# Kernel optimization log

Measured on AMD Instinct MI355X. Metric: run time of the kernel, lower is better.

Reference implementation:

```python
import jax, jax.numpy as jnp
import numpy as np

N_NODES = 64
N_EDGES = N_NODES * (N_NODES - 1)  # 4032 (fully connected, no self-loops)
BATCH = 64
N_IN = 64
N_HID = 128
N_OUT = 16


def _linear_params(key, fan_in, fan_out):
    # mimic torch nn.Linear default init: U(-1/sqrt(fan_in), 1/sqrt(fan_in))
    kw, kb = jax.random.split(key)
    s = 1.0 / np.sqrt(fan_in)
    W = jax.random.uniform(kw, (fan_in, fan_out), minval=-s, maxval=s, dtype=jnp.float32)
    b = jax.random.uniform(kb, (fan_out,), minval=-s, maxval=s, dtype=jnp.float32)
    return W, b


def setup_inputs() -> dict:
    key = jax.random.key(0)
    ks = jax.random.split(key, 10)
    # one-hot relation matrices for fully-connected graph without self loops
    pairs = np.array([(i, j) for i in range(N_NODES) for j in range(N_NODES) if i != j])
    eye = np.eye(N_NODES, dtype=np.float32)
    rel_send = jnp.asarray(eye[pairs[:, 0]])  # [E, N]
    rel_rec = jnp.asarray(eye[pairs[:, 1]])   # [E, N]

    x = jax.random.normal(ks[0], (BATCH, N_NODES, N_IN), dtype=jnp.float32)

    w1a, b1a = _linear_params(ks[1], N_IN, N_HID)
    w1b, b1b = _linear_params(ks[2], N_HID, N_HID)
    w2a, b2a = _linear_params(ks[3], 2 * N_HID, N_HID)
    w2b, b2b = _linear_params(ks[4], N_HID, N_HID)
    w3a, b3a = _linear_params(ks[5], N_HID, N_HID)
    w3b, b3b = _linear_params(ks[6], N_HID, N_HID)
    w4a, b4a = _linear_params(ks[7], 3 * N_HID, N_HID)  # factor=True
    w4b, b4b = _linear_params(ks[8], N_HID, N_HID)
    wout, bout = _linear_params(ks[9], N_HID, N_OUT)

    return dict(x=x, rel_rec=rel_rec, rel_send=rel_send,
                w1a=w1a, b1a=b1a, w1b=w1b, b1b=b1b,
                w2a=w2a, b2a=b2a, w2b=w2b, b2b=b2b,
                w3a=w3a, b3a=b3a, w3b=w3b, b3b=b3b,
                w4a=w4a, b4a=b4a, w4b=w4b, b4b=b4b,
                wout=wout, bout=bout)


def _mlp(x, wa, ba, wb, bb):
    # Linear -> ReLU -> Linear
    return jax.nn.relu(x @ wa + ba) @ wb + bb


def reference(x, rel_rec, rel_send,
              w1a, b1a, w1b, b1b,
              w2a, b2a, w2b, b2b,
              w3a, b3a, w3b, b3b,
              w4a, b4a, w4b, b4b,
              wout, bout):
    def node2edge(h):
        receivers = jnp.einsum('en,bnh->beh', rel_rec, h)
        senders = jnp.einsum('en,bnh->beh', rel_send, h)
        return jnp.concatenate([senders, receivers], axis=-1)  # [B,E,2H]

    def edge2node(e):
        agg = jnp.einsum('en,beh->bnh', rel_rec, e)
        norm = rel_rec.sum(0)[None, :, None]  # [1,N,1]
        return agg / (norm + 1e-6)

    h = _mlp(x, w1a, b1a, w1b, b1b)            # [B,N,H]
    e = _mlp(node2edge(h), w2a, b2a, w2b, b2b)  # [B,E,H]
    x_skip = e
    # factor=True branch
    n = _mlp(edge2node(e), w3a, b3a, w3b, b3b)  # [B,N,H]
    e2 = node2edge(n)                           # [B,E,2H]
    e2 = jnp.concatenate([e2, x_skip], axis=2)  # [B,E,3H]
    e2 = _mlp(e2, w4a, b4a, w4b, b4b)           # [B,E,H]
    return e2 @ wout + bout                     # [B,E,n_out]
```

## Files before the change

### kernel.cpp

```cpp
#include <hip/hip_runtime.h>
#include <hip/hip_bf16.h>


#define DI __device__ __forceinline__

typedef short bf16x8 __attribute__((ext_vector_type(8)));
typedef float f32x4 __attribute__((ext_vector_type(4)));
typedef unsigned short u16;

static constexpr int NN = 64, NE = 4032, H = 128;

DI u16 f2bf(float f) {
  union { float f; unsigned u; } v; v.f = f;
  unsigned u = v.u;
  return (u16)((u + 0x7fffu + ((u >> 16) & 1u)) >> 16);
}
DI unsigned pk2(float a, float b) {
  union { __hip_bfloat162 h; unsigned u; } c;
  c.h = __float22bfloat162_rn(float2{a, b});
  return c.u;
}
DI f32x4 mf(bf16x8 a, bf16x8 b, f32x4 c) {
  return __builtin_amdgcn_mfma_f32_16x16x32_bf16(a, b, c, 0, 0, 0);
}
DI bf16x8 ldfrag(const u16* __restrict__ p, int idx, int l) {
  return *reinterpret_cast<const bf16x8*>(p + (idx * 64 + l) * 8);
}

__global__ __launch_bounds__(64) void prepack_kernel(
    const float* __restrict__ w1a, const float* __restrict__ w1b,
    const float* __restrict__ w2a, const float* __restrict__ w2b,
    const float* __restrict__ w3a, const float* __restrict__ w3b,
    const float* __restrict__ w4a, const float* __restrict__ w4b,
    const float* __restrict__ wout,
    const float* __restrict__ b2b, const float* __restrict__ b4b,
    const float* __restrict__ bout,
    u16* __restrict__ pk, float* __restrict__ c2, float* __restrict__ c4) {
  int seg = blockIdx.y, f = blockIdx.x, l = threadIdx.x;
  int h = l >> 4, mm = l & 15;
  if (seg == 10) {
    if (f >= 4) return;
    union { u16 u[8]; uint4 q; } o;
#pragma unroll
    for (int jj = 0; jj < 8; jj++) {
      int row = f * 32 + (jj >> 2) * 16 + h * 4 + (jj & 3);
      float s = 0.f;
      for (int j = 0; j < 128; j++) s += w4b[row * 128 + j] * wout[j * 16 + mm];
      o.u[jj] = f2bf(s);
    }
    *reinterpret_cast<uint4*>(pk + ((304 + f) * 64 + l) * 8) = o.q;
    return;
  }
  if (seg == 11) {
    if (f < 2) {
      int o = f * 64 + l;
      float s = 0.f;
      for (int k = 0; k < 128; k++) s += b2b[k] * w4a[(256 + k) * 128 + o];
      c2[o] = s;
    } else if (f == 2 && l < 16) {
      float s = bout[l];
      for (int k = 0; k < 128; k++) s += b4b[k] * wout[k * 16 + l];
      c4[l] = s;
    }
    return;
  }
  const float* src; int foff, nfrag, roff, pi;
  switch (seg) {
    case 0:  src = w1a; foff = 0;   nfrag = 16; roff = 0;   pi = 0; break;
    case 1:  src = w1b; foff = 16;  nfrag = 32; roff = 0;   pi = 1; break;
    case 2:  src = w2a; foff = 48;  nfrag = 32; roff = 0;   pi = 1; break;
    case 3:  src = w2a; foff = 80;  nfrag = 32; roff = 128; pi = 1; break;
    case 4:  src = w2b; foff = 112; nfrag = 32; roff = 0;   pi = 0; break;
    case 5:  src = w3a; foff = 144; nfrag = 32; roff = 0;   pi = 1; break;
    case 6:  src = w3b; foff = 176; nfrag = 32; roff = 0;   pi = 1; break;
    case 7:  src = w4a; foff = 208; nfrag = 32; roff = 0;   pi = 1; break;
    case 8:  src = w4a; foff = 240; nfrag = 32; roff = 128; pi = 1; break;
    default: src = w4a; foff = 272; nfrag = 32; roff = 256; pi = 1; break;
  }
  if (f >= nfrag) return;
  int kt = f >> 3, ct = f & 7;
  union { u16 u[8]; uint4 q; } o;
#pragma unroll
  for (int jj = 0; jj < 8; jj++) {
    int row = pi ? (kt * 32 + (jj >> 2) * 16 + h * 4 + (jj & 3))
                 : (kt * 32 + h * 8 + jj);
    o.u[jj] = f2bf(src[(roff + row) * 128 + ct * 16 + mm]);
  }
  *reinterpret_cast<uint4*>(pk + ((foff + f) * 64 + l) * 8) = o.q;
}

__global__ __launch_bounds__(256, 4) void node_kernel(
    const float* __restrict__ x, const u16* __restrict__ pk,
    const float* __restrict__ b1a, const float* __restrict__ b1b,
    const float* __restrict__ b2a,
    float* __restrict__ sproj, float* __restrict__ rproj) {
  __shared__ bf16x8 act[2][4][64];
  int blk = blockIdx.x, b = blk >> 2, nq = blk & 3;
  int tid = threadIdx.x, l = tid & 63, w = tid >> 6;
  int m = l & 15, h = l >> 4;
  int node = nq * 16 + m;
  const f32x4 Z = {0.f, 0.f, 0.f, 0.f};
  f32x4 acc0, acc1;
  {
    const float* xb = x + (b * NN + node) * 64;
    bf16x8 xin[2];
#pragma unroll
    for (int kt = 0; kt < 2; kt++) {
      f32x4 a0 = *(const f32x4*)(xb + kt * 32 + h * 8);
      f32x4 a1 = *(const f32x4*)(xb + kt * 32 + h * 8 + 4);
      union { unsigned u[4]; bf16x8 v; } t;
      t.u[0] = pk2(a0[0], a0[1]); t.u[1] = pk2(a0[2], a0[3]);
      t.u[2] = pk2(a1[0], a1[1]); t.u[3] = pk2(a1[2], a1[3]);
      xin[kt] = t.v;
    }
#pragma unroll
    for (int kt = 0; kt < 2; kt++) {
      acc0 = mf(ldfrag(pk, kt * 8 + 2 * w, l),     xin[kt], kt == 0 ? Z : acc0);
      acc1 = mf(ldfrag(pk, kt * 8 + 2 * w + 1, l), xin[kt], kt == 0 ? Z : acc1);
    }
    f32x4 bA = *(const f32x4*)(b1a + (2 * w) * 16 + h * 4);
    f32x4 bB = *(const f32x4*)(b1a + (2 * w + 1) * 16 + h * 4);
    union { unsigned u[4]; bf16x8 v; } t;
    t.u[0] = pk2(fmaxf(acc0[0] + bA[0], 0.f), fmaxf(acc0[1] + bA[1], 0.f));
    t.u[1] = pk2(fmaxf(acc0[2] + bA[2], 0.f), fmaxf(acc0[3] + bA[3], 0.f));
    t.u[2] = pk2(fmaxf(acc1[0] + bB[0], 0.f), fmaxf(acc1[1] + bB[1], 0.f));
    t.u[3] = pk2(fmaxf(acc1[2] + bB[2], 0.f), fmaxf(acc1[3] + bB[3], 0.f));
    act[0][w][l] = t.v;
  }
  __syncthreads();
  bf16x8 ef[4];
#pragma unroll
  for (int kt = 0; kt < 4; kt++) ef[kt] = act[0][kt][l];
#pragma unroll
  for (int kt = 0; kt < 4; kt++) {
    acc0 = mf(ldfrag(pk + 16 * 512, kt * 8 + 2 * w, l),     ef[kt], kt == 0 ? Z : acc0);
    acc1 = mf(ldfrag(pk + 16 * 512, kt * 8 + 2 * w + 1, l), ef[kt], kt == 0 ? Z : acc1);
  }
  {
    f32x4 bA = *(const f32x4*)(b1b + (2 * w) * 16 + h * 4);
    f32x4 bB = *(const f32x4*)(b1b + (2 * w + 1) * 16 + h * 4);
    union { unsigned u[4]; bf16x8 v; } t;
    t.u[0] = pk2(acc0[0] + bA[0], acc0[1] + bA[1]);
    t.u[1] = pk2(acc0[2] + bA[2], acc0[3] + bA[3]);
    t.u[2] = pk2(acc1[0] + bB[0], acc1[1] + bB[1]);
    t.u[3] = pk2(acc1[2] + bB[2], acc1[3] + bB[3]);
    act[1][w][l] = t.v;
  }
  __syncthreads();
#pragma unroll
  for (int kt = 0; kt < 4; kt++) ef[kt] = act[1][kt][l];
#pragma unroll
  for (int kt = 0; kt < 4; kt++) {
    acc0 = mf(ldfrag(pk + 48 * 512, kt * 8 + 2 * w, l),     ef[kt], kt == 0 ? Z : acc0);
    acc1 = mf(ldfrag(pk + 48 * 512, kt * 8 + 2 * w + 1, l), ef[kt], kt == 0 ? Z : acc1);
  }
  float* spo = sproj + (b * NN + node) * H;
  *reinterpret_cast<f32x4*>(spo + (2 * w) * 16 + h * 4) = acc0;
  *reinterpret_cast<f32x4*>(spo + (2 * w + 1) * 16 + h * 4) = acc1;
#pragma unroll
  for (int kt = 0; kt < 4; kt++) {
    acc0 = mf(ldfrag(pk + 80 * 512, kt * 8 + 2 * w, l),     ef[kt], kt == 0 ? Z : acc0);
    acc1 = mf(ldfrag(pk + 80 * 512, kt * 8 + 2 * w + 1, l), ef[kt], kt == 0 ? Z : acc1);
  }
  {
    f32x4 bA = *(const f32x4*)(b2a + (2 * w) * 16 + h * 4);
    f32x4 bB = *(const f32x4*)(b2a + (2 * w + 1) * 16 + h * 4);
    float* rpo = rproj + (b * NN + node) * H;
    f32x4 o0 = acc0, o1 = acc1;
    o0[0] += bA[0]; o0[1] += bA[1]; o0[2] += bA[2]; o0[3] += bA[3];
    o1[0] += bB[0]; o1[1] += bB[1]; o1[2] += bB[2]; o1[3] += bB[3];
    *reinterpret_cast<f32x4*>(rpo + (2 * w) * 16 + h * 4) = o0;
    *reinterpret_cast<f32x4*>(rpo + (2 * w + 1) * 16 + h * 4) = o1;
  }
}

__global__ __launch_bounds__(256, 3) void agg_kernel(
    const float* __restrict__ sproj, const float* __restrict__ rproj,
    const u16* __restrict__ pk,
    const float* __restrict__ b2b, const float* __restrict__ b3a,
    const float* __restrict__ b3b, const float* __restrict__ b4a,
    const float* __restrict__ c2,
    float* __restrict__ s4, float* __restrict__ r4) {
  __shared__ f32x4 lred[4][8][64];
  __shared__ bf16x8 act[2][4][64];
  int blk = blockIdx.x, b = blk >> 2, jq = blk & 3;
  int tid = threadIdx.x, l = tid & 63, w = tid >> 6, m = l & 15, h = l >> 4;
  int j = jq * 16 + m;
  const float* rpb = rproj + (b * NN + j) * H;
  f32x4 rpv[8], accS[8];
#pragma unroll
  for (int k = 0; k < 8; k++) {
    rpv[k] = *(const f32x4*)(rpb + (k >> 1) * 32 + h * 8 + (k & 1) * 4);
    accS[k] = f32x4{0.f, 0.f, 0.f, 0.f};
  }
  const float* spb = sproj + b * NN * H;
  for (int i = w * 16; i < w * 16 + 16; i++) {
    const float* sp = spb + i * H;
#pragma unroll
    for (int k = 0; k < 8; k++) {
      f32x4 s = *(const f32x4*)(sp + (k >> 1) * 32 + h * 8 + (k & 1) * 4);
      f32x4 t = s + rpv[k];
      t[0] = fmaxf(t[0], 0.f); t[1] = fmaxf(t[1], 0.f);
      t[2] = fmaxf(t[2], 0.f); t[3] = fmaxf(t[3], 0.f);
      accS[k] += t;
    }
  }
  if (w == jq) {
    const float* sp = spb + j * H;
#pragma unroll
    for (int k = 0; k < 8; k++) {
      f32x4 s = *(const f32x4*)(sp + (k >> 1) * 32 + h * 8 + (k & 1) * 4);
      f32x4 t = s + rpv[k];
      accS[k][0] -= fmaxf(t[0], 0.f); accS[k][1] -= fmaxf(t[1], 0.f);
      accS[k][2] -= fmaxf(t[2], 0.f); accS[k][3] -= fmaxf(t[3], 0.f);
    }
  }
#pragma unroll
  for (int k = 0; k < 8; k++) lred[w][k][l] = accS[k];
  __syncthreads();
  {
    f32x4 s0 = lred[0][2 * w][l] + lred[1][2 * w][l] + lred[2][2 * w][l] + lred[3][2 * w][l];
    f32x4 s1 = lred[0][2 * w + 1][l] + lred[1][2 * w + 1][l] + lred[2][2 * w + 1][l] + lred[3][2 * w + 1][l];
    union { unsigned u[4]; bf16x8 v; } t;
    t.u[0] = pk2(s0[0], s0[1]); t.u[1] = pk2(s0[2], s0[3]);
    t.u[2] = pk2(s1[0], s1[1]); t.u[3] = pk2(s1[2], s1[3]);
    act[0][w][l] = t.v;
  }
  __syncthreads();
  const f32x4 Z = {0.f, 0.f, 0.f, 0.f};
  f32x4 acc0, acc1;
  bf16x8 ef[4];
#pragma unroll
  for (int kt = 0; kt < 4; kt++) ef[kt] = act[0][kt][l];
#pragma unroll
  for (int kt = 0; kt < 4; kt++) {
    acc0 = mf(ldfrag(pk + 112 * 512, kt * 8 + 2 * w, l),     ef[kt], kt == 0 ? Z : acc0);
    acc1 = mf(ldfrag(pk + 112 * 512, kt * 8 + 2 * w + 1, l), ef[kt], kt == 0 ? Z : acc1);
  }
  {
    const float inv = 1.0f / (63.0f + 1e-6f);
    const float binv = 63.0f * inv;
    f32x4 bA = *(const f32x4*)(b2b + (2 * w) * 16 + h * 4);
    f32x4 bB = *(const f32x4*)(b2b + (2 * w + 1) * 16 + h * 4);
    union { unsigned u[4]; bf16x8 v; } t;
    t.u[0] = pk2(acc0[0] * inv + bA[0] * binv, acc0[1] * inv + bA[1] * binv);
    t.u[1] = pk2(acc0[2] * inv + bA[2] * binv, acc0[3] * inv + bA[3] * binv);
    t.u[2] = pk2(acc1[0] * inv + bB[0] * binv, acc1[1] * inv + bB[1] * binv);
    t.u[3] = pk2(acc1[2] * inv + bB[2] * binv, acc1[3] * inv + bB[3] * binv);
    act[1][w][l] = t.v;
  }
  __syncthreads();
#pragma unroll
  for (int kt = 0; kt < 4; kt++) ef[kt] = act[1][kt][l];
#pragma unroll
  for (int kt = 0; kt < 4; kt++) {
    acc0 = mf(ldfrag(pk + 144 * 512, kt * 8 + 2 * w, l),     ef[kt], kt == 0 ? Z : acc0);
    acc1 = mf(ldfrag(pk + 144 * 512, kt * 8 + 2 * w + 1, l), ef[kt], kt == 0 ? Z : acc1);
  }
  {
    f32x4 bA = *(const f32x4*)(b3a + (2 * w) * 16 + h * 4);
    f32x4 bB = *(const f32x4*)(b3a + (2 * w + 1) * 16 + h * 4);
    union { unsigned u[4]; bf16x8 v; } t;
    t.u[0] = pk2(fmaxf(acc0[0] + bA[0], 0.f), fmaxf(acc0[1] + bA[1], 0.f));
    t.u[1] = pk2(fmaxf(acc0[2] + bA[2], 0.f), fmaxf(acc0[3] + bA[3], 0.f));
    t.u[2] = pk2(fmaxf(acc1[0] + bB[0], 0.f), fmaxf(acc1[1] + bB[1], 0.f));
    t.u[3] = pk2(fmaxf(acc1[2] + bB[2], 0.f), fmaxf(acc1[3] + bB[3], 0.f));
    act[0][w][l] = t.v;
  }
  __syncthreads();
#pragma unroll
  for (int kt = 0; kt < 4; kt++) ef[kt] = act[0][kt][l];
#pragma unroll
  for (int kt = 0; kt < 4; kt++) {
    acc0 = mf(ldfrag(pk + 176 * 512, kt * 8 + 2 * w, l),     ef[kt], kt == 0 ? Z : acc0);
    acc1 = mf(ldfrag(pk + 176 * 512, kt * 8 + 2 * w + 1, l), ef[kt], kt == 0 ? Z : acc1);
  }
  {
    f32x4 bA = *(const f32x4*)(b3b + (2 * w) * 16 + h * 4);
    f32x4 bB = *(const f32x4*)(b3b + (2 * w + 1) * 16 + h * 4);
    union { unsigned u[4]; bf16x8 v; } t;
    t.u[0] = pk2(acc0[0] + bA[0], acc0[1] + bA[1]);
    t.u[1] = pk2(acc0[2] + bA[2], acc0[3] + bA[3]);
    t.u[2] = pk2(acc1[0] + bB[0], acc1[1] + bB[1]);
    t.u[3] = pk2(acc1[2] + bB[2], acc1[3] + bB[3]);
    act[1][w][l] = t.v;
  }
  __syncthreads();
#pragma unroll
  for (int kt = 0; kt < 4; kt++) ef[kt] = act[1][kt][l];
#pragma unroll
  for (int kt = 0; kt < 4; kt++) {
    acc0 = mf(ldfrag(pk + 208 * 512, kt * 8 + 2 * w, l),     ef[kt], kt == 0 ? Z : acc0);
    acc1 = mf(ldfrag(pk + 208 * 512, kt * 8 + 2 * w + 1, l), ef[kt], kt == 0 ? Z : acc1);
  }
  {
    f32x4 cA = *(const f32x4*)(c2 + (2 * w) * 16 + h * 4);
    f32x4 cB = *(const f32x4*)(c2 + (2 * w + 1) * 16 + h * 4);
    float* s4o = s4 + (b * NN + j) * H;
    f32x4 o0 = acc0, o1 = acc1;
    o0[0] += cA[0]; o0[1] += cA[1]; o0[2] += cA[2]; o0[3] += cA[3];
    o1[0] += cB[0]; o1[1] += cB[1]; o1[2] += cB[2]; o1[3] += cB[3];
    *reinterpret_cast<f32x4*>(s4o + (2 * w) * 16 + h * 4) = o0;
    *reinterpret_cast<f32x4*>(s4o + (2 * w + 1) * 16 + h * 4) = o1;
  }
#pragma unroll
  for (int kt = 0; kt < 4; kt++) {
    acc0 = mf(ldfrag(pk + 240 * 512, kt * 8 + 2 * w, l),     ef[kt], kt == 0 ? Z : acc0);
    acc1 = mf(ldfrag(pk + 240 * 512, kt * 8 + 2 * w + 1, l), ef[kt], kt == 0 ? Z : acc1);
  }
  {
    f32x4 bA = *(const f32x4*)(b4a + (2 * w) * 16 + h * 4);
    f32x4 bB = *(const f32x4*)(b4a + (2 * w + 1) * 16 + h * 4);
    float* r4o = r4 + (b * NN + j) * H;
    f32x4 o0 = acc0, o1 = acc1;
    o0[0] += bA[0]; o0[1] += bA[1]; o0[2] += bA[2]; o0[3] += bA[3];
    o1[0] += bB[0]; o1[1] += bB[1]; o1[2] += bB[2]; o1[3] += bB[3];
    *reinterpret_cast<f32x4*>(r4o + (2 * w) * 16 + h * 4) = o0;
    *reinterpret_cast<f32x4*>(r4o + (2 * w + 1) * 16 + h * 4) = o1;
  }
}

__global__ __launch_bounds__(256, 3) void edge_kernel(
    const float* __restrict__ sproj, const float* __restrict__ rproj,
    const float* __restrict__ s4, const float* __restrict__ r4,
    const u16* __restrict__ pk, const float* __restrict__ c4,
    float* __restrict__ out) {
  __shared__ alignas(16) u16 wl[32 * 512];
  int blk = blockIdx.x;
  int b = blk >> 5, sg = blk & 31;
  int tid = threadIdx.x, l = tid & 63, w = tid >> 6;
  int m = l & 15, h = l >> 4;
  int i = sg * 2 + (w >> 1);
  int hf = w & 1;
#pragma unroll
  for (int it = 0; it < 8; it++) {
    int idx = it * 256 + tid;
    *reinterpret_cast<uint4*>(&wl[idx * 8]) =
        *reinterpret_cast<const uint4*>(pk + 112 * 512 + idx * 8);
  }
  const float* sp  = sproj + (b * NN + i) * H;
  const float* rpb = rproj + b * NN * H;
  int jn[2];
#pragma unroll
  for (int mt = 0; mt < 2; mt++) {
    int jj = (hf * 2 + mt) * 16 + m;
    int v = jj + (jj >= i ? 1 : 0); jn[mt] = v > 63 ? 63 : v;
  }
  __syncthreads();
  const f32x4 Z = {0.f, 0.f, 0.f, 0.f};
  f32x4 acc[2][8];
  bf16x8 ef[2][4];
#pragma unroll
  for (int kt = 0; kt < 4; kt++) {
    f32x4 s0 = *(const f32x4*)(sp + kt * 32 + h * 8);
    f32x4 s1 = *(const f32x4*)(sp + kt * 32 + h * 8 + 4);
    bf16x8 tb[2];
#pragma unroll
    for (int mt = 0; mt < 2; mt++) {
      const float* rp = rpb + jn[mt] * H;
      f32x4 r0 = *(const f32x4*)(rp + kt * 32 + h * 8);
      f32x4 r1 = *(const f32x4*)(rp + kt * 32 + h * 8 + 4);
      union { unsigned u[4]; bf16x8 v; } t;
      t.u[0] = pk2(fmaxf(r0[0] + s0[0], 0.f), fmaxf(r0[1] + s0[1], 0.f));
      t.u[1] = pk2(fmaxf(r0[2] + s0[2], 0.f), fmaxf(r0[3] + s0[3], 0.f));
      t.u[2] = pk2(fmaxf(r1[0] + s1[0], 0.f), fmaxf(r1[1] + s1[1], 0.f));
      t.u[3] = pk2(fmaxf(r1[2] + s1[2], 0.f), fmaxf(r1[3] + s1[3], 0.f));
      tb[mt] = t.v;
    }
#pragma unroll
    for (int ft = 0; ft < 8; ft++) {
      bf16x8 wv = *reinterpret_cast<const bf16x8*>(&wl[((kt * 8 + ft) * 64 + l) * 8]);
#pragma unroll
      for (int mt = 0; mt < 2; mt++)
        acc[mt][ft] = mf(wv, tb[mt], kt == 0 ? Z : acc[mt][ft]);
    }
  }
#pragma unroll
  for (int mt = 0; mt < 2; mt++)
#pragma unroll
    for (int k2 = 0; k2 < 4; k2++) {
      f32x4 a0 = acc[mt][2 * k2], a1 = acc[mt][2 * k2 + 1];
      union { unsigned u[4]; bf16x8 v; } t2;
      t2.u[0] = pk2(a0[0], a0[1]); t2.u[1] = pk2(a0[2], a0[3]);
      t2.u[2] = pk2(a1[0], a1[1]); t2.u[3] = pk2(a1[2], a1[3]);
      ef[mt][k2] = t2.v;
    }
  __syncthreads();
#pragma unroll
  for (int it = 0; it < 8; it++) {
    int idx = it * 256 + tid;
    *reinterpret_cast<uint4*>(&wl[idx * 8]) =
        *reinterpret_cast<const uint4*>(pk + 272 * 512 + idx * 8);
  }
  __syncthreads();
#pragma unroll
  for (int kt = 0; kt < 4; kt++)
#pragma unroll
    for (int ft = 0; ft < 8; ft++) {
      bf16x8 wv = *reinterpret_cast<const bf16x8*>(&wl[((kt * 8 + ft) * 64 + l) * 8]);
#pragma unroll
      for (int mt = 0; mt < 2; mt++)
        acc[mt][ft] = mf(wv, ef[mt][kt], kt == 0 ? Z : acc[mt][ft]);
    }
  {
    const float* s4p = s4 + (b * NN + i) * H;
    const float* r4b = r4 + b * NN * H;
#pragma unroll
    for (int k2 = 0; k2 < 4; k2++) {
      f32x4 sA = *(const f32x4*)(s4p + (2 * k2) * 16 + h * 4);
      f32x4 sB = *(const f32x4*)(s4p + (2 * k2 + 1) * 16 + h * 4);
#pragma unroll
      for (int mt = 0; mt < 2; mt++) {
        const float* r4p = r4b + jn[mt] * H;
        f32x4 rA = *(const f32x4*)(r4p + (2 * k2) * 16 + h * 4);
        f32x4 rB = *(const f32x4*)(r4p + (2 * k2 + 1) * 16 + h * 4);
        f32x4 a0 = acc[mt][2 * k2], a1 = acc[mt][2 * k2 + 1];
        union { unsigned u[4]; bf16x8 v; } t2;
        t2.u[0] = pk2(fmaxf(a0[0] + sA[0] + rA[0], 0.f), fmaxf(a0[1] + sA[1] + rA[1], 0.f));
        t2.u[1] = pk2(fmaxf(a0[2] + sA[2] + rA[2], 0.f), fmaxf(a0[3] + sA[3] + rA[3], 0.f));
        t2.u[2] = pk2(fmaxf(a1[0] + sB[0] + rB[0], 0.f), fmaxf(a1[1] + sB[1] + rB[1], 0.f));
        t2.u[3] = pk2(fmaxf(a1[2] + sB[2] + rB[2], 0.f), fmaxf(a1[3] + sB[3] + rB[3], 0.f));
        ef[mt][k2] = t2.v;
      }
    }
  }
  {
    bf16x8 wfv[4];
#pragma unroll
    for (int i2 = 0; i2 < 4; i2++) wfv[i2] = ldfrag(pk + 304 * 512, i2, l);
    f32x4 c4v = *(const f32x4*)(c4 + h * 4);
#pragma unroll
    for (int mt = 0; mt < 2; mt++) {
      f32x4 a4 = Z;
#pragma unroll
      for (int kt = 0; kt < 4; kt++) a4 = mf(wfv[kt], ef[mt][kt], a4);
      int jj = (hf * 2 + mt) * 16 + m;
      if (jj < 63) {
        f32x4 o;
        o[0] = a4[0] + c4v[0]; o[1] = a4[1] + c4v[1];
        o[2] = a4[2] + c4v[2]; o[3] = a4[3] + c4v[3];
        *reinterpret_cast<f32x4*>(out + (b * NE + i * 63 + jj) * 16 + h * 4) = o;
      }
    }
  }
}

extern "C" void kernel_launch(void* const* d_in, const int* in_sizes, int n_in,
                              void* d_out, int out_size, void* d_ws, size_t ws_size,
                              hipStream_t stream) {
  const float* x    = (const float*)d_in[0];
  const float* w1a  = (const float*)d_in[3];
  const float* b1a  = (const float*)d_in[4];
  const float* w1b  = (const float*)d_in[5];
  const float* b1b  = (const float*)d_in[6];
  const float* w2a  = (const float*)d_in[7];
  const float* b2a  = (const float*)d_in[8];
  const float* w2b  = (const float*)d_in[9];
  const float* b2b  = (const float*)d_in[10];
  const float* w3a  = (const float*)d_in[11];
  const float* b3a  = (const float*)d_in[12];
  const float* w3b  = (const float*)d_in[13];
  const float* b3b  = (const float*)d_in[14];
  const float* w4a  = (const float*)d_in[15];
  const float* b4a  = (const float*)d_in[16];
  const float* w4b  = (const float*)d_in[17];
  const float* b4b  = (const float*)d_in[18];
  const float* wout = (const float*)d_in[19];
  const float* bout = (const float*)d_in[20];
  float* out = (float*)d_out;

  float* sproj = (float*)d_ws;
  float* rproj = sproj + 524288;
  float* s4    = rproj + 524288;
  float* r4    = s4 + 524288;
  u16* pkw     = (u16*)(r4 + 524288);
  float* c2    = (float*)(pkw + 174080);
  float* c4    = c2 + 128;

  prepack_kernel<<<dim3(32, 12), 64, 0, stream>>>(
      w1a, w1b, w2a, w2b, w3a, w3b, w4a, w4b, wout, b2b, b4b, bout, pkw, c2, c4);
  node_kernel<<<256, 256, 0, stream>>>(x, pkw, b1a, b1b, b2a, sproj, rproj);
  agg_kernel<<<256, 256, 0, stream>>>(sproj, rproj, pkw, b2b, b3a, b3b, b4a, c2, s4, r4);
  edge_kernel<<<2048, 256, 0, stream>>>(sproj, rproj, s4, r4, pkw, c4, out);
}
```

Before: 101.2 us.

## Split edge kernel work by output-feature columns per wave, stage activations in LDS

The edge kernel now assigns one sender node per block, with each of the four waves owning 32 output features across all 64 receivers. Each wave keeps its weight fragments in registers loaded straight from global memory instead of copying the full weight matrix into shared memory, and intermediate activations are exchanged through two small LDS buffers. Prepack layouts for two weight segments change to match the new fragment ordering. The grid doubles and occupancy bound rises, at the cost of extra LDS round trips and barriers between layers.

After: 94.25 us. 1.07x faster.

```diff
diff --git a/kernel.cpp b/kernel.cpp
--- a/kernel.cpp
+++ b/kernel.cpp
@@ -43,7 +43,7 @@
     union { u16 u[8]; uint4 q; } o;
 #pragma unroll
     for (int jj = 0; jj < 8; jj++) {
-      int row = f * 32 + (jj >> 2) * 16 + h * 4 + (jj & 3);
+      int row = f * 32 + h * 8 + jj;
       float s = 0.f;
       for (int j = 0; j < 128; j++) s += w4b[row * 128 + j] * wout[j * 16 + mm];
       o.u[jj] = f2bf(s);
@@ -75,7 +75,7 @@
     case 6:  src = w3b; foff = 176; nfrag = 32; roff = 0;   pi = 1; break;
     case 7:  src = w4a; foff = 208; nfrag = 32; roff = 0;   pi = 1; break;
     case 8:  src = w4a; foff = 240; nfrag = 32; roff = 128; pi = 1; break;
-    default: src = w4a; foff = 272; nfrag = 32; roff = 256; pi = 1; break;
+    default: src = w4a; foff = 272; nfrag = 32; roff = 256; pi = 0; break;
   }
   if (f >= nfrag) return;
   int kt = f >> 3, ct = f & 7;
@@ -320,127 +320,128 @@
   }
 }
 
-__global__ __launch_bounds__(256, 3) void edge_kernel(
+__global__ __launch_bounds__(256, 4) void edge_kernel(
     const float* __restrict__ sproj, const float* __restrict__ rproj,
     const float* __restrict__ s4, const float* __restrict__ r4,
     const u16* __restrict__ pk, const float* __restrict__ c4,
     float* __restrict__ out) {
-  __shared__ alignas(16) u16 wl[32 * 512];
+  __shared__ alignas(16) u16 bufA[8192];
+  __shared__ alignas(16) u16 bufB[8192];
   int blk = blockIdx.x;
-  int b = blk >> 5, sg = blk & 31;
+  int b = blk >> 6, i = blk & 63;
   int tid = threadIdx.x, l = tid & 63, w = tid >> 6;
-  int m = l & 15, h = l >> 4;
-  int i = sg * 2 + (w >> 1);
-  int hf = w & 1;
-#pragma unroll
-  for (int it = 0; it < 8; it++) {
-    int idx = it * 256 + tid;
-    *reinterpret_cast<uint4*>(&wl[idx * 8]) =
-        *reinterpret_cast<const uint4*>(pk + 112 * 512 + idx * 8);
-  }
-  const float* sp  = sproj + (b * NN + i) * H;
-  const float* rpb = rproj + b * NN * H;
-  int jn[2];
-#pragma unroll
-  for (int mt = 0; mt < 2; mt++) {
-    int jj = (hf * 2 + mt) * 16 + m;
-    int v = jj + (jj >= i ? 1 : 0); jn[mt] = v > 63 ? 63 : v;
-  }
-  __syncthreads();
+  int m16 = l & 15, h = l >> 4;
   const f32x4 Z = {0.f, 0.f, 0.f, 0.f};
-  f32x4 acc[2][8];
-  bf16x8 ef[2][4];
-#pragma unroll
-  for (int kt = 0; kt < 4; kt++) {
-    f32x4 s0 = *(const f32x4*)(sp + kt * 32 + h * 8);
-    f32x4 s1 = *(const f32x4*)(sp + kt * 32 + h * 8 + 4);
-    bf16x8 tb[2];
-#pragma unroll
-    for (int mt = 0; mt < 2; mt++) {
-      const float* rp = rpb + jn[mt] * H;
-      f32x4 r0 = *(const f32x4*)(rp + kt * 32 + h * 8);
-      f32x4 r1 = *(const f32x4*)(rp + kt * 32 + h * 8 + 4);
-      union { unsigned u[4]; bf16x8 v; } t;
-      t.u[0] = pk2(fmaxf(r0[0] + s0[0], 0.f), fmaxf(r0[1] + s0[1], 0.f));
-      t.u[1] = pk2(fmaxf(r0[2] + s0[2], 0.f), fmaxf(r0[3] + s0[3], 0.f));
-      t.u[2] = pk2(fmaxf(r1[0] + s1[0], 0.f), fmaxf(r1[1] + s1[1], 0.f));
-      t.u[3] = pk2(fmaxf(r1[2] + s1[2], 0.f), fmaxf(r1[3] + s1[3], 0.f));
-      tb[mt] = t.v;
-    }
-#pragma unroll
-    for (int ft = 0; ft < 8; ft++) {
-      bf16x8 wv = *reinterpret_cast<const bf16x8*>(&wl[((kt * 8 + ft) * 64 + l) * 8]);
-#pragma unroll
-      for (int mt = 0; mt < 2; mt++)
-        acc[mt][ft] = mf(wv, tb[mt], kt == 0 ? Z : acc[mt][ft]);
-    }
-  }
-#pragma unroll
-  for (int mt = 0; mt < 2; mt++)
-#pragma unroll
-    for (int k2 = 0; k2 < 4; k2++) {
-      f32x4 a0 = acc[mt][2 * k2], a1 = acc[mt][2 * k2 + 1];
-      union { unsigned u[4]; bf16x8 v; } t2;
-      t2.u[0] = pk2(a0[0], a0[1]); t2.u[1] = pk2(a0[2], a0[3]);
-      t2.u[2] = pk2(a1[0], a1[1]); t2.u[3] = pk2(a1[2], a1[3]);
-      ef[mt][k2] = t2.v;
-    }
-  __syncthreads();
-#pragma unroll
-  for (int it = 0; it < 8; it++) {
-    int idx = it * 256 + tid;
-    *reinterpret_cast<uint4*>(&wl[idx * 8]) =
-        *reinterpret_cast<const uint4*>(pk + 272 * 512 + idx * 8);
-  }
-  __syncthreads();
-#pragma unroll
-  for (int kt = 0; kt < 4; kt++)
-#pragma unroll
-    for (int ft = 0; ft < 8; ft++) {
-      bf16x8 wv = *reinterpret_cast<const bf16x8*>(&wl[((kt * 8 + ft) * 64 + l) * 8]);
-#pragma unroll
-      for (int mt = 0; mt < 2; mt++)
-        acc[mt][ft] = mf(wv, ef[mt][kt], kt == 0 ? Z : acc[mt][ft]);
-    }
-  {
-    const float* s4p = s4 + (b * NN + i) * H;
-    const float* r4b = r4 + b * NN * H;
-#pragma unroll
-    for (int k2 = 0; k2 < 4; k2++) {
-      f32x4 sA = *(const f32x4*)(s4p + (2 * k2) * 16 + h * 4);
-      f32x4 sB = *(const f32x4*)(s4p + (2 * k2 + 1) * 16 + h * 4);
-#pragma unroll
-      for (int mt = 0; mt < 2; mt++) {
-        const float* r4p = r4b + jn[mt] * H;
-        f32x4 rA = *(const f32x4*)(r4p + (2 * k2) * 16 + h * 4);
-        f32x4 rB = *(const f32x4*)(r4p + (2 * k2 + 1) * 16 + h * 4);
-        f32x4 a0 = acc[mt][2 * k2], a1 = acc[mt][2 * k2 + 1];
-        union { unsigned u[4]; bf16x8 v; } t2;
-        t2.u[0] = pk2(fmaxf(a0[0] + sA[0] + rA[0], 0.f), fmaxf(a0[1] + sA[1] + rA[1], 0.f));
-        t2.u[1] = pk2(fmaxf(a0[2] + sA[2] + rA[2], 0.f), fmaxf(a0[3] + sA[3] + rA[3], 0.f));
-        t2.u[2] = pk2(fmaxf(a1[0] + sB[0] + rB[0], 0.f), fmaxf(a1[1] + sB[1] + rB[1], 0.f));
-        t2.u[3] = pk2(fmaxf(a1[2] + sB[2] + rB[2], 0.f), fmaxf(a1[3] + sB[3] + rB[3], 0.f));
-        ef[mt][k2] = t2.v;
+  int jnv[4];
+#pragma unroll
+  for (int n = 0; n < 4; n++) {
+    int e = n * 16 + m16;
+    int v = e + (e >= i ? 1 : 0); jnv[n] = v > 63 ? 63 : v;
+  }
+  {
+    const float* spp = sproj + (b * NN + i) * H + w * 32 + h * 8;
+    f32x4 s0 = *(const f32x4*)spp, s1 = *(const f32x4*)(spp + 4);
+#pragma unroll
+    for (int n = 0; n < 4; n++) {
+      const float* rpp = rproj + (b * NN + jnv[n]) * H + w * 32 + h * 8;
+      f32x4 r0 = *(const f32x4*)rpp, r1 = *(const f32x4*)(rpp + 4);
+      union { unsigned u[4]; uint4 q; } t;
+      t.u[0] = pk2(fmaxf(s0[0] + r0[0], 0.f), fmaxf(s0[1] + r0[1], 0.f));
+      t.u[1] = pk2(fmaxf(s0[2] + r0[2], 0.f), fmaxf(s0[3] + r0[3], 0.f));
+      t.u[2] = pk2(fmaxf(s1[0] + r1[0], 0.f), fmaxf(s1[1] + r1[1], 0.f));
+      t.u[3] = pk2(fmaxf(s1[2] + r1[2], 0.f), fmaxf(s1[3] + r1[3], 0.f));
+      *reinterpret_cast<uint4*>(&bufA[((w * 4 + n) * 64 + l) * 8]) = t.q;
+    }
+  }
+  bf16x8 wv[8];
+#pragma unroll
+  for (int idx = 0; idx < 8; idx++)
+    wv[idx] = ldfrag(pk + 112 * 512, (idx >> 1) * 8 + 2 * w + (idx & 1), l);
+  __syncthreads();
+  f32x4 acc[2][4];
+#pragma unroll
+  for (int n = 0; n < 4; n++) {
+    bf16x8 bf[4];
+#pragma unroll
+    for (int kt = 0; kt < 4; kt++)
+      bf[kt] = *reinterpret_cast<const bf16x8*>(&bufA[((kt * 4 + n) * 64 + l) * 8]);
+#pragma unroll
+    for (int kt = 0; kt < 4; kt++)
+#pragma unroll
+      for (int m = 0; m < 2; m++)
+        acc[m][n] = mf(wv[kt * 2 + m], bf[kt], kt == 0 ? Z : acc[m][n]);
+  }
+#pragma unroll
+  for (int idx = 0; idx < 8; idx++)
+    wv[idx] = ldfrag(pk + 272 * 512, (idx >> 1) * 8 + 2 * w + (idx & 1), l);
+  {
+    int lane2b = (h >> 1) * 16 + m16;
+    int jb = (h & 1) * 4;
+#pragma unroll
+    for (int m = 0; m < 2; m++)
+#pragma unroll
+      for (int n = 0; n < 4; n++) {
+        union { unsigned u[2]; unsigned long long d; } p;
+        p.u[0] = pk2(acc[m][n][0], acc[m][n][1]);
+        p.u[1] = pk2(acc[m][n][2], acc[m][n][3]);
+        *reinterpret_cast<unsigned long long*>(
+            &bufB[((w * 4 + n) * 64 + lane2b + m * 32) * 8 + jb]) = p.d;
       }
-    }
-  }
-  {
-    bf16x8 wfv[4];
-#pragma unroll
-    for (int i2 = 0; i2 < 4; i2++) wfv[i2] = ldfrag(pk + 304 * 512, i2, l);
-    f32x4 c4v = *(const f32x4*)(c4 + h * 4);
-#pragma unroll
-    for (int mt = 0; mt < 2; mt++) {
-      f32x4 a4 = Z;
-#pragma unroll
-      for (int kt = 0; kt < 4; kt++) a4 = mf(wfv[kt], ef[mt][kt], a4);
-      int jj = (hf * 2 + mt) * 16 + m;
-      if (jj < 63) {
-        f32x4 o;
-        o[0] = a4[0] + c4v[0]; o[1] = a4[1] + c4v[1];
-        o[2] = a4[2] + c4v[2]; o[3] = a4[3] + c4v[3];
-        *reinterpret_cast<f32x4*>(out + (b * NE + i * 63 + jj) * 16 + h * 4) = o;
+  }
+  __syncthreads();
+#pragma unroll
+  for (int n = 0; n < 4; n++) {
+    bf16x8 bf[4];
+#pragma unroll
+    for (int kt = 0; kt < 4; kt++)
+      bf[kt] = *reinterpret_cast<const bf16x8*>(&bufB[((kt * 4 + n) * 64 + l) * 8]);
+#pragma unroll
+    for (int kt = 0; kt < 4; kt++)
+#pragma unroll
+      for (int m = 0; m < 2; m++)
+        acc[m][n] = mf(wv[kt * 2 + m], bf[kt], kt == 0 ? Z : acc[m][n]);
+  }
+  {
+    f32x4 s4v[2];
+#pragma unroll
+    for (int m = 0; m < 2; m++)
+      s4v[m] = *(const f32x4*)(s4 + (b * NN + i) * H + w * 32 + m * 16 + h * 4);
+    int lane2b = (h >> 1) * 16 + m16;
+    int jb = (h & 1) * 4;
+#pragma unroll
+    for (int n = 0; n < 4; n++) {
+      const float* r4p = r4 + (b * NN + jnv[n]) * H + w * 32 + h * 4;
+#pragma unroll
+      for (int m = 0; m < 2; m++) {
+        f32x4 rv = *(const f32x4*)(r4p + m * 16);
+        union { unsigned u[2]; unsigned long long d; } p;
+        p.u[0] = pk2(fmaxf(acc[m][n][0] + s4v[m][0] + rv[0], 0.f),
+                     fmaxf(acc[m][n][1] + s4v[m][1] + rv[1], 0.f));
+        p.u[1] = pk2(fmaxf(acc[m][n][2] + s4v[m][2] + rv[2], 0.f),
+                     fmaxf(acc[m][n][3] + s4v[m][3] + rv[3], 0.f));
+        *reinterpret_cast<unsigned long long*>(
+            &bufA[((w * 4 + n) * 64 + lane2b + m * 32) * 8 + jb]) = p.d;
       }
+    }
+  }
+  __syncthreads();
+  {
+    bf16x8 wfv[4], bf[4];
+#pragma unroll
+    for (int kt = 0; kt < 4; kt++) {
+      wfv[kt] = ldfrag(pk + 304 * 512, kt, l);
+      bf[kt] = *reinterpret_cast<const bf16x8*>(&bufA[((kt * 4 + w) * 64 + l) * 8]);
+    }
+    f32x4 a4 = Z;
+#pragma unroll
+    for (int kt = 0; kt < 4; kt++) a4 = mf(wfv[kt], bf[kt], a4);
+    int jj = w * 16 + m16;
+    if (jj < 63) {
+      f32x4 c4v = *(const f32x4*)(c4 + h * 4);
+      f32x4 o;
+      o[0] = a4[0] + c4v[0]; o[1] = a4[1] + c4v[1];
+      o[2] = a4[2] + c4v[2]; o[3] = a4[3] + c4v[3];
+      *reinterpret_cast<f32x4*>(out + (b * NE + i * 63 + jj) * 16 + h * 4) = o;
     }
   }
 }
@@ -481,5 +482,5 @@
       w1a, w1b, w2a, w2b, w3a, w3b, w4a, w4b, wout, b2b, b4b, bout, pkw, c2, c4);
   node_kernel<<<256, 256, 0, stream>>>(x, pkw, b1a, b1b, b2a, sproj, rproj);
   agg_kernel<<<256, 256, 0, stream>>>(sproj, rproj, pkw, b2b, b3a, b3b, b4a, c2, s4, r4);
-  edge_kernel<<<2048, 256, 0, stream>>>(sproj, rproj, s4, r4, pkw, c4, out);
-}
+  edge_kernel<<<4096, 256, 0, stream>>>(sproj, rproj, s4, r4, pkw, c4, out);
+}
```
